# Performance work log

Measured on AMD Instinct MI355X. Metric: run time of the kernel, lower is better.

The kernel has to match this reference:

```python
import jax, jax.numpy as jnp
import numpy as np

B, C, H, W = 32, 64, 56, 56
REPN, NK, SMALL = 50, 17, 3   # repN=64-int(64*0.23), nk=ceil(51/3)
GROUPS = 4                     # N_rep
EPS = 1e-5


def _build_index_mats():
    """Reduce the fallback's python scatter-add loops to exact linear maps.
    For flat position p=r*NK+j the roll shifts depend only on p%3, so each
    shift class s gets a (REPN,NK) count matrix over source nk-slots."""
    rng = np.random.RandomState(123)
    ghost = np.sort(rng.choice(C, C - REPN, replace=False))
    rep = np.array(sorted(set(range(C)) - set(ghost.tolist())), np.int32)
    Mh = np.zeros((3, REPN, NK), np.int32)
    Mv = np.zeros((3, REPN, NK), np.int32)
    Mid = np.zeros((REPN, NK), np.int32)
    for _ in range(GROUPS):
        for r in range(REPN):
            perm = rng.permutation(NK)
            for p in range(NK):
                Mh[(r * NK + p) % 3, r, perm[p]] += 1
        for r in range(REPN):
            perm = rng.permutation(NK)
            for p in range(NK):
                Mv[(r * NK + p) % 3, r, perm[p]] += 1
        kk = rng.randint(0, NK, REPN)
        for r in range(REPN):
            Mid[r, kk[r]] += 1
    return ghost.astype(np.int32), rep, Mh, Mv, Mid


def setup_inputs() -> dict:
    key = jax.random.key(0)
    k1, k2, k3 = jax.random.split(key, 3)
    ghost, rep, Mh, Mv, Mid = _build_index_mats()
    return {
        "inputs": jax.random.normal(k1, (B, C, H, W), jnp.float32),
        "w0": jax.random.normal(k2, (REPN * NK, 1, SMALL, SMALL), jnp.float32) * 0.1,
        "w1": jax.random.normal(k3, (REPN * NK, 1, SMALL, SMALL), jnp.float32) * 0.1,
        "Mh": jnp.asarray(Mh), "Mv": jnp.asarray(Mv), "Mid": jnp.asarray(Mid),
        "ghost_idx": jnp.asarray(ghost), "rep_idx": jnp.asarray(rep),
    }


def _bn(x):
    # BatchNorm2d in training mode, affine weight=1 / bias=0 (init values)
    m = x.mean(axis=(0, 2, 3), keepdims=True)
    v = x.var(axis=(0, 2, 3), keepdims=True)
    return (x - m) / jnp.sqrt(v + EPS)


def reference(inputs, w0, w1, Mh, Mv, Mid, ghost_idx, rep_idx):
    rep_in = inputs[:, rep_idx]      # (B, REPN, H, W)
    ghost_in = inputs[:, ghost_idx]  # (B, ghostN, H, W)

    def conv(w):  # depthwise-grouped conv: groups=REPN, each 1->NK channels
        return jax.lax.conv_general_dilated(
            rep_in, w, window_strides=(1, 1), padding=((2, 2), (2, 2)),
            dimension_numbers=('NCHW', 'OIHW', 'NCHW'),
            feature_group_count=REPN)

    out = conv(w0) + conv(w1)                       # (B, REPN*NK, H+2, W+2)
    xv = out.reshape(B, REPN, NK, H + 2, W + 2)

    Mhf, Mvf, Midf = (m.astype(xv.dtype) for m in (Mh, Mv, Mid))
    sh1, sw1 = (0, 1, 2), (0, 2, 1)   # lora1: shifts (i%3, 2i%3)
    sh2, sw2 = (0, 2, 1), (0, 1, 2)   # lora2: shifts (2i%3, i%3)

    lora1 = sum(jnp.roll(jnp.einsum('rk,brkhw->brhw', Mhf[s], xv),
                         (sh1[s], sw1[s]), axis=(2, 3)) for s in range(3))
    lora2 = sum(jnp.roll(jnp.einsum('rk,brkhw->brhw', Mvf[s], xv),
                         (sh2[s], sw2[s]), axis=(2, 3)) for s in range(3))
    small = jnp.einsum('rk,brkhw->brhw', Midf, xv)

    # center-crop back to (H, W): dh = dw = 1
    lora1 = lora1[:, :, 1:1 + H, 1:1 + W]
    lora2 = lora2[:, :, 1:1 + H, 1:1 + W]
    small = small[:, :, 1:1 + H, 1:1 + W]

    x = _bn(lora1) + _bn(lora2) + _bn(small) + rep_in
    return jnp.concatenate([x, ghost_in], axis=1)   # (B, C, H, W)
```

## Files before the change

kernel.cpp:

```cpp
#include <hip/hip_runtime.h>
#include <hip/hip_cooperative_groups.h>

namespace cg = cooperative_groups;

#define Bn 32
#define Cn 64
#define Hn 56
#define Wn 56
#define REPN 50
#define NKn 17
#define HWn (Hn*Wn)
#define NSTATf 100352.0f
#define EPSf 1e-5f

#define PART_OFF 0
#define WEFF_OFF 9600

#define SEGH 7
#define NTASK 112

__device__ __forceinline__ void weff_one(int idx,
        const float* __restrict__ w0, const float* __restrict__ w1,
        const int* __restrict__ Mh, const int* __restrict__ Mv,
        const int* __restrict__ Mid, float* __restrict__ ws)
{
    int r   = idx / 63;
    int rem = idx % 63;
    int t   = rem / 9;
    int ij  = rem % 9;
    const int* M = (t < 3) ? (Mh + (t*REPN + r)*NKn)
                 : (t < 6) ? (Mv + ((t-3)*REPN + r)*NKn)
                           : (Mid + r*NKn);
    float acc = 0.f;
    #pragma unroll
    for (int k = 0; k < NKn; ++k)
        acc += (float)M[k] * (w0[(r*NKn + k)*9 + ij] + w1[(r*NKn + k)*9 + ij]);
    ws[WEFF_OFF + idx] = acc;
}

__global__ void k_weff(const float* __restrict__ w0, const float* __restrict__ w1,
                       const int* __restrict__ Mh, const int* __restrict__ Mv,
                       const int* __restrict__ Mid, float* __restrict__ ws)
{
    int idx = blockIdx.x * blockDim.x + threadIdx.x;
    if (idx < REPN*63) weff_one(idx, w0, w1, Mh, Mv, Mid, ws);
}

__device__ __forceinline__ void load_row8c(const float* __restrict__ ch, int row, int q,
                                           float* __restrict__ X, float& c55)
{
    bool rv = (row >= 0) && (row < Hn);
    int rc = rv ? row : 0;
    const float* rp = ch + rc*Wn;
    float4 c0 = *(const float4*)(rp + (q ? 4*q - 4 : 0));
    float4 c1 = *(const float4*)(rp + 4*q);
    int ox = (4*q + 4 <= 55) ? 4*q + 4 : 55;
    float cx = rp[ox];
    float mr = rv ? 1.f : 0.f;
    float m0 = (rv && q > 0)  ? 1.f : 0.f;
    float mx = (rv && q < 13) ? 1.f : 0.f;
    X[0]=c0.y*m0; X[1]=c0.z*m0; X[2]=c0.w*m0;
    X[3]=c1.x*mr; X[4]=c1.y*mr; X[5]=c1.z*mr; X[6]=c1.w*mr;
    X[7]=cx*mx;
    c55 = (q == 0) ? rp[55]*mr : 0.f;
}

template <typename F>
__device__ __forceinline__ void conv_walk(const float* __restrict__ ch,
        const float (&wk)[63], int tid, F emit)
{
    if (tid >= NTASK) return;
    int seg = tid / 14;
    int q   = tid - seg*14;
    int h0  = seg * SEGH;
    bool top = (seg == 0);

    float W[5][8], C[5], T[8];
    {
        float dummy;
        if (top) load_row8c(ch, 55, q, T, dummy);
    }
    #pragma unroll
    for (int k = 0; k < 5; ++k)
        load_row8c(ch, h0 - 3 + k, q, W[k], C[k]);

    #pragma unroll
    for (int s = 0; s < SEGH; ++s) {
        int h = h0 + s;
        float Wn8[8], Cn1;
        load_row8c(ch, h + 2, q, Wn8, Cn1);

        float l1[4], l2[4], sm[4];
        #pragma unroll
        for (int p = 0; p < 4; ++p) { l1[p]=0.f; l2[p]=0.f; sm[p]=0.f; }
        #pragma unroll
        for (int i = 0; i < 3; ++i)
            #pragma unroll
            for (int j = 0; j < 3; ++j) {
                float wh0 = wk[i*3+j],    wv0 = wk[27+i*3+j], wid = wk[54+i*3+j];
                float wh1 = wk[9+i*3+j],  wv2 = wk[45+i*3+j];
                float wh2 = wk[18+i*3+j], wv1 = wk[36+i*3+j];
                #pragma unroll
                for (int p = 0; p < 4; ++p) {
                    float a  = W[2+i][p+2+j];
                    l1[p] = fmaf(a, wh0, l1[p]);
                    l2[p] = fmaf(a, wv0, l2[p]);
                    sm[p] = fmaf(a, wid, sm[p]);
                    float bA = W[1+i][p+j];
                    l1[p] = fmaf(bA, wh1, l1[p]);
                    l2[p] = fmaf(bA, wv2, l2[p]);
                    float bB = W[i][p+1+j];
                    l1[p] = fmaf(bB, wh2, l1[p]);
                    l2[p] = fmaf(bB, wv1, l2[p]);
                }
            }
        if (q == 0) {
            #pragma unroll
            for (int i = 0; i < 3; ++i) {
                l1[0] = fmaf(C[1+i], wk[9+3*i],  l1[0]);
                l2[0] = fmaf(C[1+i], wk[45+3*i], l2[0]);
            }
        }
        if (s == 0 && top) {
            #pragma unroll
            for (int j = 0; j < 3; ++j)
                #pragma unroll
                for (int p = 0; p < 4; ++p) {
                    l1[p] = fmaf(T[p+1+j], wk[18+j], l1[p]);
                    l2[p] = fmaf(T[p+1+j], wk[36+j], l2[p]);
                }
        }
        float res[4] = {W[3][3], W[3][4], W[3][5], W[3][6]};
        emit(h, q, l1, l2, sm, res);

        #pragma unroll
        for (int k = 0; k < 4; ++k) {
            #pragma unroll
            for (int x = 0; x < 8; ++x) W[k][x] = W[k+1][x];
            C[k] = C[k+1];
        }
        #pragma unroll
        for (int x = 0; x < 8; ++x) W[4][x] = Wn8[x];
        C[4] = Cn1;
    }
}

__global__ void __launch_bounds__(128, 2) k_fused(const float* __restrict__ in,
        const float* __restrict__ w0, const float* __restrict__ w1,
        const int* __restrict__ Mh, const int* __restrict__ Mv,
        const int* __restrict__ Mid,
        const int* __restrict__ rep_idx, const int* __restrict__ ghost_idx,
        float* __restrict__ ws, float* __restrict__ out)
{
    cg::grid_group grid = cg::this_grid();
    int tid = threadIdx.x;

    {
        int gidx = blockIdx.x * 128 + tid;
        if (gidx < REPN*63) weff_one(gidx, w0, w1, Mh, Mv, Mid, ws);
    }
    grid.sync();

    __shared__ float red[2][6];
    #pragma unroll
    for (int it = 0; it < 2; ++it) {
        int v = blockIdx.x*2 + it;
        int c = v & 63;
        int b = v >> 6;
        if (c >= REPN) {
            int cin = ghost_idx[c - REPN];
            const float4* s4 = (const float4*)(in + ((size_t)(b*Cn + cin))*HWn);
            float4* d4 = (float4*)(out + ((size_t)(b*Cn + c))*HWn);
            for (int i = tid; i < HWn/4; i += 128) d4[i] = s4[i];
            continue;
        }
        int r = c;
        const float* wr = ws + WEFF_OFF + r*63;
        float wk[63];
        #pragma unroll
        for (int i = 0; i < 63; ++i) wk[i] = wr[i];
        const float* ch = in + ((size_t)(b*Cn + rep_idx[r]))*HWn;

        float s1=0.f,q1=0.f,s2=0.f,q2=0.f,s3=0.f,q3=0.f;
        conv_walk(ch, wk, tid,
            [&](int h, int q, float* l1, float* l2, float* sm, float* res) {
                (void)h; (void)q; (void)res;
                #pragma unroll
                for (int p = 0; p < 4; ++p) {
                    s1 += l1[p]; q1 += l1[p]*l1[p];
                    s2 += l2[p]; q2 += l2[p]*l2[p];
                    s3 += sm[p]; q3 += sm[p]*sm[p];
                }
            });
        __syncthreads();
        {
            float vals[6] = {s1,q1,s2,q2,s3,q3};
            int lane = tid & 63, wave = tid >> 6;
            #pragma unroll
            for (int x = 0; x < 6; ++x) {
                float y = vals[x];
                for (int o = 32; o; o >>= 1) y += __shfl_down(y, o, 64);
                if (lane == 0) red[wave][x] = y;
            }
        }
        __syncthreads();
        if (tid < 6)
            ws[PART_OFF + (tid*REPN + r)*Bn + b] = red[0][tid] + red[1][tid];
    }
    grid.sync();

    __shared__ float sred[6];
    #pragma unroll
    for (int it = 0; it < 2; ++it) {
        int v = blockIdx.x*2 + it;
        int c = v & 63;
        int b = v >> 6;
        if (c >= REPN) continue;
        int r = c;
        __syncthreads();
        if (tid < 6) {
            const float* pp = ws + PART_OFF + (tid*REPN + r)*Bn;
            float s = 0.f;
            #pragma unroll
            for (int i = 0; i < Bn; ++i) s += pp[i];
            sred[tid] = s;
        }
        __syncthreads();
        const float inv = 1.0f / NSTATf;
        float m1 = sred[0]*inv, v1 = sred[1]*inv - m1*m1;
        float m2 = sred[2]*inv, v2 = sred[3]*inv - m2*m2;
        float m3 = sred[4]*inv, v3 = sred[5]*inv - m3*m3;
        float r1 = rsqrtf(v1 + EPSf), r2 = rsqrtf(v2 + EPSf), r3 = rsqrtf(v3 + EPSf);

        const float* wr = ws + WEFF_OFF + r*63;
        float wk[63];
        #pragma unroll
        for (int i = 0; i < 63; ++i) wk[i] = wr[i];
        const float* ch = in + ((size_t)(b*Cn + rep_idx[r]))*HWn;
        float* dst = out + ((size_t)(b*Cn + c))*HWn;

        conv_walk(ch, wk, tid,
            [&](int h, int q, float* l1, float* l2, float* sm, float* res) {
                float4 o;
                o.x = (l1[0]-m1)*r1 + (l2[0]-m2)*r2 + (sm[0]-m3)*r3 + res[0];
                o.y = (l1[1]-m1)*r1 + (l2[1]-m2)*r2 + (sm[1]-m3)*r3 + res[1];
                o.z = (l1[2]-m1)*r1 + (l2[2]-m2)*r2 + (sm[2]-m3)*r3 + res[2];
                o.w = (l1[3]-m1)*r1 + (l2[3]-m2)*r2 + (sm[3]-m3)*r3 + res[3];
                *(float4*)(dst + h*Wn + 4*q) = o;
            });
    }
}

__global__ void __launch_bounds__(128) k_stats(const float* __restrict__ in,
        const int* __restrict__ rep_idx, float* __restrict__ ws)
{
    int bid = blockIdx.x;
    int r = bid % REPN;
    int b = bid / REPN;
    int tid = threadIdx.x;

    const float* wr = ws + WEFF_OFF + r*63;
    float wk[63];
    #pragma unroll
    for (int i = 0; i < 63; ++i) wk[i] = wr[i];
    const float* ch = in + ((size_t)(b*Cn + rep_idx[r]))*HWn;

    float s1=0.f,q1=0.f,s2=0.f,q2=0.f,s3=0.f,q3=0.f;
    conv_walk(ch, wk, tid,
        [&](int h, int q, float* l1, float* l2, float* sm, float* res) {
            (void)h; (void)q; (void)res;
            #pragma unroll
            for (int p = 0; p < 4; ++p) {
                s1 += l1[p]; q1 += l1[p]*l1[p];
                s2 += l2[p]; q2 += l2[p]*l2[p];
                s3 += sm[p]; q3 += sm[p]*sm[p];
            }
        });

    __shared__ float red[2][6];
    float vals[6] = {s1,q1,s2,q2,s3,q3};
    int lane = tid & 63, wave = tid >> 6;
    #pragma unroll
    for (int v = 0; v < 6; ++v) {
        float x = vals[v];
        for (int o = 32; o; o >>= 1) x += __shfl_down(x, o, 64);
        if (lane == 0) red[wave][v] = x;
    }
    __syncthreads();
    if (tid < 6)
        ws[PART_OFF + (tid*REPN + r)*Bn + b] = red[0][tid] + red[1][tid];
}

__global__ void __launch_bounds__(128) k_out(const float* __restrict__ in,
        const int* __restrict__ rep_idx, const int* __restrict__ ghost_idx,
        const float* __restrict__ ws, float* __restrict__ out)
{
    int bid = blockIdx.x;
    int c = bid % Cn;
    int b = bid / Cn;
    int tid = threadIdx.x;

    if (c >= REPN) {
        int cin = ghost_idx[c - REPN];
        const float4* s4 = (const float4*)(in + ((size_t)(b*Cn + cin))*HWn);
        float4* d4 = (float4*)(out + ((size_t)(b*Cn + c))*HWn);
        for (int i = tid; i < HWn/4; i += 128) d4[i] = s4[i];
        return;
    }

    int r = c;
    __shared__ float sred[6];
    if (tid < 6) {
        const float* pp = ws + PART_OFF + (tid*REPN + r)*Bn;
        float s = 0.f;
        #pragma unroll
        for (int i = 0; i < Bn; ++i) s += pp[i];
        sred[tid] = s;
    }
    __syncthreads();
    const float inv = 1.0f / NSTATf;
    float m1 = sred[0]*inv, v1 = sred[1]*inv - m1*m1;
    float m2 = sred[2]*inv, v2 = sred[3]*inv - m2*m2;
    float m3 = sred[4]*inv, v3 = sred[5]*inv - m3*m3;
    float r1 = rsqrtf(v1 + EPSf), r2 = rsqrtf(v2 + EPSf), r3 = rsqrtf(v3 + EPSf);

    const float* wr = ws + WEFF_OFF + r*63;
    float wk[63];
    #pragma unroll
    for (int i = 0; i < 63; ++i) wk[i] = wr[i];
    const float* ch = in + ((size_t)(b*Cn + rep_idx[r]))*HWn;
    float* dst = out + ((size_t)(b*Cn + c))*HWn;

    conv_walk(ch, wk, tid,
        [&](int h, int q, float* l1, float* l2, float* sm, float* res) {
            float4 o;
            o.x = (l1[0]-m1)*r1 + (l2[0]-m2)*r2 + (sm[0]-m3)*r3 + res[0];
            o.y = (l1[1]-m1)*r1 + (l2[1]-m2)*r2 + (sm[1]-m3)*r3 + res[1];
            o.z = (l1[2]-m1)*r1 + (l2[2]-m2)*r2 + (sm[2]-m3)*r3 + res[2];
            o.w = (l1[3]-m1)*r1 + (l2[3]-m2)*r2 + (sm[3]-m3)*r3 + res[3];
            *(float4*)(dst + h*Wn + 4*q) = o;
        });
}

extern "C" void kernel_launch(void* const* d_in, const int* in_sizes, int n_in,
                              void* d_out, int out_size, void* d_ws, size_t ws_size,
                              hipStream_t stream) {
    const float* in   = (const float*)d_in[0];
    const float* w0   = (const float*)d_in[1];
    const float* w1   = (const float*)d_in[2];
    const int*   Mh   = (const int*)d_in[3];
    const int*   Mv   = (const int*)d_in[4];
    const int*   Mid  = (const int*)d_in[5];
    const int*   ghost= (const int*)d_in[6];
    const int*   rep  = (const int*)d_in[7];
    float* out  = (float*)d_out;
    float* ws   = (float*)d_ws;

    int maxBlk = 0;
    hipError_t qerr = hipOccupancyMaxActiveBlocksPerMultiprocessor(
        &maxBlk, (const void*)k_fused, 128, 0);
    bool coop_ok = (qerr == hipSuccess) && (maxBlk >= 4);

    if (coop_ok) {
        void* args[] = { (void*)&in, (void*)&w0, (void*)&w1, (void*)&Mh,
                         (void*)&Mv, (void*)&Mid, (void*)&rep, (void*)&ghost,
                         (void*)&ws, (void*)&out };
        hipError_t lerr = hipLaunchCooperativeKernel((const void*)k_fused,
                              dim3(1024), dim3(128), args, 0, stream);
        if (lerr == hipSuccess) return;
    }
    k_weff<<<(REPN*63 + 127)/128, 128, 0, stream>>>(w0, w1, Mh, Mv, Mid, ws);
    k_stats<<<Bn*REPN, 128, 0, stream>>>(in, rep, ws);
    k_out<<<Bn*Cn, 128, 0, stream>>>(in, rep, ghost, ws, out);
}
```

Baseline: 124.2 us.

## Move folded conv weights to shared memory and launch one block per plane

Repacks the effective 3x3 weights into a padded 8-wide interleaved layout in shared memory, read as float4 pairs, instead of holding 63 weights in registers. This cuts register pressure so launch bounds can rise to 4 blocks per SIMD group, and the cooperative grid doubles to 2048 blocks, one (batch, channel) plane each. Ghost-channel copies now run before the first grid sync. The cost is LDS reads inside the inner loop and a stricter occupancy requirement (8 blocks per CU) for the cooperative path, otherwise it falls back to three separate kernels.

```diff
diff --git a/kernel.cpp b/kernel.cpp
--- a/kernel.cpp
+++ b/kernel.cpp
@@ -15,19 +15,22 @@
 
 #define PART_OFF 0
 #define WEFF_OFF 9600
+#define WEFF_N   (REPN*72)
 
 #define SEGH 7
 #define NTASK 112
+#define GRID_FUSED 2048
 
 __device__ __forceinline__ void weff_one(int idx,
         const float* __restrict__ w0, const float* __restrict__ w1,
         const int* __restrict__ Mh, const int* __restrict__ Mv,
         const int* __restrict__ Mid, float* __restrict__ ws)
 {
-    int r   = idx / 63;
-    int rem = idx % 63;
-    int t   = rem / 9;
-    int ij  = rem % 9;
+    int r   = idx / 72;
+    int rem = idx % 72;
+    int ij  = rem >> 3;
+    int t   = rem & 7;
+    if (t == 7) { ws[WEFF_OFF + idx] = 0.f; return; }
     const int* M = (t < 3) ? (Mh + (t*REPN + r)*NKn)
                  : (t < 6) ? (Mv + ((t-3)*REPN + r)*NKn)
                            : (Mid + r*NKn);
@@ -43,7 +46,7 @@
                        const int* __restrict__ Mid, float* __restrict__ ws)
 {
     int idx = blockIdx.x * blockDim.x + threadIdx.x;
-    if (idx < REPN*63) weff_one(idx, w0, w1, Mh, Mv, Mid, ws);
+    if (idx < WEFF_N) weff_one(idx, w0, w1, Mh, Mv, Mid, ws);
 }
 
 __device__ __forceinline__ void load_row8c(const float* __restrict__ ch, int row, int q,
@@ -67,7 +70,7 @@
 
 template <typename F>
 __device__ __forceinline__ void conv_walk(const float* __restrict__ ch,
-        const float (&wk)[63], int tid, F emit)
+        const float* __restrict__ swk, int tid, F emit)
 {
     if (tid >= NTASK) return;
     int seg = tid / 14;
@@ -90,6 +93,10 @@
         float Wn8[8], Cn1;
         load_row8c(ch, h + 2, q, Wn8, Cn1);
 
+        int z = 0;
+        asm volatile("" : "+v"(z));
+        const float* wz = swk + z;
+
         float l1[4], l2[4], sm[4];
         #pragma unroll
         for (int p = 0; p < 4; ++p) { l1[p]=0.f; l2[p]=0.f; sm[p]=0.f; }
@@ -97,9 +104,11 @@
         for (int i = 0; i < 3; ++i)
             #pragma unroll
             for (int j = 0; j < 3; ++j) {
-                float wh0 = wk[i*3+j],    wv0 = wk[27+i*3+j], wid = wk[54+i*3+j];
-                float wh1 = wk[9+i*3+j],  wv2 = wk[45+i*3+j];
-                float wh2 = wk[18+i*3+j], wv1 = wk[36+i*3+j];
+                int ij = i*3 + j;
+                float4 wa = *(const float4*)(wz + ij*8);
+                float4 wb = *(const float4*)(wz + ij*8 + 4);
+                float wh0 = wa.x, wh1 = wa.y, wh2 = wa.z, wv0 = wa.w;
+                float wv1 = wb.x, wv2 = wb.y, wid = wb.z;
                 #pragma unroll
                 for (int p = 0; p < 4; ++p) {
                     float a  = W[2+i][p+2+j];
@@ -117,8 +126,8 @@
         if (q == 0) {
             #pragma unroll
             for (int i = 0; i < 3; ++i) {
-                l1[0] = fmaf(C[1+i], wk[9+3*i],  l1[0]);
-                l2[0] = fmaf(C[1+i], wk[45+3*i], l2[0]);
+                l1[0] = fmaf(C[1+i], wz[(3*i)*8 + 1], l1[0]);
+                l2[0] = fmaf(C[1+i], wz[(3*i)*8 + 5], l2[0]);
             }
         }
         if (s == 0 && top) {
@@ -126,8 +135,8 @@
             for (int j = 0; j < 3; ++j)
                 #pragma unroll
                 for (int p = 0; p < 4; ++p) {
-                    l1[p] = fmaf(T[p+1+j], wk[18+j], l1[p]);
-                    l2[p] = fmaf(T[p+1+j], wk[36+j], l2[p]);
+                    l1[p] = fmaf(T[p+1+j], wz[j*8 + 2], l1[p]);
+                    l2[p] = fmaf(T[p+1+j], wz[j*8 + 4], l2[p]);
                 }
         }
         float res[4] = {W[3][3], W[3][4], W[3][5], W[3][6]};
@@ -145,7 +154,7 @@
     }
 }
 
-__global__ void __launch_bounds__(128, 2) k_fused(const float* __restrict__ in,
+__global__ void __launch_bounds__(128, 4) k_fused(const float* __restrict__ in,
         const float* __restrict__ w0, const float* __restrict__ w1,
         const int* __restrict__ Mh, const int* __restrict__ Mv,
         const int* __restrict__ Mid,
@@ -154,35 +163,35 @@
 {
     cg::grid_group grid = cg::this_grid();
     int tid = threadIdx.x;
+    int v = blockIdx.x;
+    int c = v & 63;
+    int b = v >> 6;
+    bool ghost = (c >= REPN);
+
+    __shared__ float swk[72];
+    __shared__ float red[2][6];
+    __shared__ float sred[6];
 
     {
         int gidx = blockIdx.x * 128 + tid;
-        if (gidx < REPN*63) weff_one(gidx, w0, w1, Mh, Mv, Mid, ws);
+        if (gidx < WEFF_N) weff_one(gidx, w0, w1, Mh, Mv, Mid, ws);
+    }
+    if (ghost) {
+        int cin = ghost_idx[c - REPN];
+        const float4* s4 = (const float4*)(in + ((size_t)(b*Cn + cin))*HWn);
+        float4* d4 = (float4*)(out + ((size_t)(b*Cn + c))*HWn);
+        for (int i = tid; i < HWn/4; i += 128) d4[i] = s4[i];
     }
     grid.sync();
 
-    __shared__ float red[2][6];
-    #pragma unroll
-    for (int it = 0; it < 2; ++it) {
-        int v = blockIdx.x*2 + it;
-        int c = v & 63;
-        int b = v >> 6;
-        if (c >= REPN) {
-            int cin = ghost_idx[c - REPN];
-            const float4* s4 = (const float4*)(in + ((size_t)(b*Cn + cin))*HWn);
-            float4* d4 = (float4*)(out + ((size_t)(b*Cn + c))*HWn);
-            for (int i = tid; i < HWn/4; i += 128) d4[i] = s4[i];
-            continue;
-        }
+    if (!ghost) {
         int r = c;
-        const float* wr = ws + WEFF_OFF + r*63;
-        float wk[63];
-        #pragma unroll
-        for (int i = 0; i < 63; ++i) wk[i] = wr[i];
+        if (tid < 72) swk[tid] = ws[WEFF_OFF + r*72 + tid];
+        __syncthreads();
         const float* ch = in + ((size_t)(b*Cn + rep_idx[r]))*HWn;
 
         float s1=0.f,q1=0.f,s2=0.f,q2=0.f,s3=0.f,q3=0.f;
-        conv_walk(ch, wk, tid,
+        conv_walk(ch, swk, tid,
             [&](int h, int q, float* l1, float* l2, float* sm, float* res) {
                 (void)h; (void)q; (void)res;
                 #pragma unroll
@@ -192,7 +201,6 @@
                     s3 += sm[p]; q3 += sm[p]*sm[p];
                 }
             });
-        __syncthreads();
         {
             float vals[6] = {s1,q1,s2,q2,s3,q3};
             int lane = tid & 63, wave = tid >> 6;
@@ -205,50 +213,38 @@
         }
         __syncthreads();
         if (tid < 6)
-            ws[PART_OFF + (tid*REPN + r)*Bn + b] = red[0][tid] + red[1][tid];
+            ws[PART_OFF + (tid*REPN + c)*Bn + b] = red[0][tid] + red[1][tid];
     }
     grid.sync();
 
-    __shared__ float sred[6];
-    #pragma unroll
-    for (int it = 0; it < 2; ++it) {
-        int v = blockIdx.x*2 + it;
-        int c = v & 63;
-        int b = v >> 6;
-        if (c >= REPN) continue;
-        int r = c;
-        __syncthreads();
-        if (tid < 6) {
-            const float* pp = ws + PART_OFF + (tid*REPN + r)*Bn;
-            float s = 0.f;
-            #pragma unroll
-            for (int i = 0; i < Bn; ++i) s += pp[i];
-            sred[tid] = s;
-        }
-        __syncthreads();
-        const float inv = 1.0f / NSTATf;
-        float m1 = sred[0]*inv, v1 = sred[1]*inv - m1*m1;
-        float m2 = sred[2]*inv, v2 = sred[3]*inv - m2*m2;
-        float m3 = sred[4]*inv, v3 = sred[5]*inv - m3*m3;
-        float r1 = rsqrtf(v1 + EPSf), r2 = rsqrtf(v2 + EPSf), r3 = rsqrtf(v3 + EPSf);
-
-        const float* wr = ws + WEFF_OFF + r*63;
-        float wk[63];
-        #pragma unroll
-        for (int i = 0; i < 63; ++i) wk[i] = wr[i];
-        const float* ch = in + ((size_t)(b*Cn + rep_idx[r]))*HWn;
-        float* dst = out + ((size_t)(b*Cn + c))*HWn;
-
-        conv_walk(ch, wk, tid,
-            [&](int h, int q, float* l1, float* l2, float* sm, float* res) {
-                float4 o;
-                o.x = (l1[0]-m1)*r1 + (l2[0]-m2)*r2 + (sm[0]-m3)*r3 + res[0];
-                o.y = (l1[1]-m1)*r1 + (l2[1]-m2)*r2 + (sm[1]-m3)*r3 + res[1];
-                o.z = (l1[2]-m1)*r1 + (l2[2]-m2)*r2 + (sm[2]-m3)*r3 + res[2];
-                o.w = (l1[3]-m1)*r1 + (l2[3]-m2)*r2 + (sm[3]-m3)*r3 + res[3];
-                *(float4*)(dst + h*Wn + 4*q) = o;
-            });
-    }
+    if (ghost) return;
+    int r = c;
+    if (tid < 6) {
+        const float* pp = ws + PART_OFF + (tid*REPN + r)*Bn;
+        float s = 0.f;
+        #pragma unroll
+        for (int i = 0; i < Bn; ++i) s += pp[i];
+        sred[tid] = s;
+    }
+    __syncthreads();
+    const float inv = 1.0f / NSTATf;
+    float m1 = sred[0]*inv, v1 = sred[1]*inv - m1*m1;
+    float m2 = sred[2]*inv, v2 = sred[3]*inv - m2*m2;
+    float m3 = sred[4]*inv, v3 = sred[5]*inv - m3*m3;
+    float r1 = rsqrtf(v1 + EPSf), r2 = rsqrtf(v2 + EPSf), r3 = rsqrtf(v3 + EPSf);
+
+    const float* ch = in + ((size_t)(b*Cn + rep_idx[r]))*HWn;
+    float* dst = out + ((size_t)(b*Cn + c))*HWn;
+
+    conv_walk(ch, swk, tid,
+        [&](int h, int q, float* l1, float* l2, float* sm, float* res) {
+            float4 o;
+            o.x = (l1[0]-m1)*r1 + (l2[0]-m2)*r2 + (sm[0]-m3)*r3 + res[0];
+            o.y = (l1[1]-m1)*r1 + (l2[1]-m2)*r2 + (sm[1]-m3)*r3 + res[1];
+            o.z = (l1[2]-m1)*r1 + (l2[2]-m2)*r2 + (sm[2]-m3)*r3 + res[2];
+            o.w = (l1[3]-m1)*r1 + (l2[3]-m2)*r2 + (sm[3]-m3)*r3 + res[3];
+            *(float4*)(dst + h*Wn + 4*q) = o;
+        });
 }
 
 __global__ void __launch_bounds__(128) k_stats(const float* __restrict__ in,
@@ -259,14 +255,13 @@
     int b = bid / REPN;
     int tid = threadIdx.x;
 
-    const float* wr = ws + WEFF_OFF + r*63;
-    float wk[63];
-    #pragma unroll
-    for (int i = 0; i < 63; ++i) wk[i] = wr[i];
+    __shared__ float swk[72];
+    if (tid < 72) swk[tid] = ws[WEFF_OFF + r*72 + tid];
+    __syncthreads();
     const float* ch = in + ((size_t)(b*Cn + rep_idx[r]))*HWn;
 
     float s1=0.f,q1=0.f,s2=0.f,q2=0.f,s3=0.f,q3=0.f;
-    conv_walk(ch, wk, tid,
+    conv_walk(ch, swk, tid,
         [&](int h, int q, float* l1, float* l2, float* sm, float* res) {
             (void)h; (void)q; (void)res;
             #pragma unroll
@@ -309,7 +304,9 @@
     }
 
     int r = c;
+    __shared__ float swk[72];
     __shared__ float sred[6];
+    if (tid < 72) swk[tid] = ws[WEFF_OFF + r*72 + tid];
     if (tid < 6) {
         const float* pp = ws + PART_OFF + (tid*REPN + r)*Bn;
         float s = 0.f;
@@ -324,14 +321,10 @@
     float m3 = sred[4]*inv, v3 = sred[5]*inv - m3*m3;
     float r1 = rsqrtf(v1 + EPSf), r2 = rsqrtf(v2 + EPSf), r3 = rsqrtf(v3 + EPSf);
 
-    const float* wr = ws + WEFF_OFF + r*63;
-    float wk[63];
-    #pragma unroll
-    for (int i = 0; i < 63; ++i) wk[i] = wr[i];
     const float* ch = in + ((size_t)(b*Cn + rep_idx[r]))*HWn;
     float* dst = out + ((size_t)(b*Cn + c))*HWn;
 
-    conv_walk(ch, wk, tid,
+    conv_walk(ch, swk, tid,
         [&](int h, int q, float* l1, float* l2, float* sm, float* res) {
             float4 o;
             o.x = (l1[0]-m1)*r1 + (l2[0]-m2)*r2 + (sm[0]-m3)*r3 + res[0];
@@ -359,17 +352,17 @@
     int maxBlk = 0;
     hipError_t qerr = hipOccupancyMaxActiveBlocksPerMultiprocessor(
         &maxBlk, (const void*)k_fused, 128, 0);
-    bool coop_ok = (qerr == hipSuccess) && (maxBlk >= 4);
+    bool coop_ok = (qerr == hipSuccess) && (maxBlk >= 8);
 
     if (coop_ok) {
         void* args[] = { (void*)&in, (void*)&w0, (void*)&w1, (void*)&Mh,
                          (void*)&Mv, (void*)&Mid, (void*)&rep, (void*)&ghost,
                          (void*)&ws, (void*)&out };
         hipError_t lerr = hipLaunchCooperativeKernel((const void*)k_fused,
-                              dim3(1024), dim3(128), args, 0, stream);
+                              dim3(GRID_FUSED), dim3(128), args, 0, stream);
         if (lerr == hipSuccess) return;
     }
-    k_weff<<<(REPN*63 + 127)/128, 128, 0, stream>>>(w0, w1, Mh, Mv, Mid, ws);
+    k_weff<<<(WEFF_N + 127)/128, 128, 0, stream>>>(w0, w1, Mh, Mv, Mid, ws);
     k_stats<<<Bn*REPN, 128, 0, stream>>>(in, rep, ws);
     k_out<<<Bn*Cn, 128, 0, stream>>>(in, rep, ghost, ws, out);
 }
```

Measured after the change: 133.4 us. +7.4%, slower.

## Replace cooperative kernel with two passes and fold BN into combined conv weights

Applied to the files above, without the earlier changes.

Removes the cooperative grid-synced kernel and its separate weight-combination pass. Each block now computes its own effective 3x3 weights into shared memory. The output pass folds the three batch-norm scalings into a single set of three shifted-kernel weights plus a constant, so it runs one convolution accumulation instead of three. This trades grid-wide syncs and one extra launch for redundant per-block weight computation and two regular launches, and it cuts the FMA count in the output pass.

```diff
diff --git a/kernel.cpp b/kernel.cpp
--- a/kernel.cpp
+++ b/kernel.cpp
@@ -1,7 +1,4 @@
 #include <hip/hip_runtime.h>
-#include <hip/hip_cooperative_groups.h>
-
-namespace cg = cooperative_groups;
 
 #define Bn 32
 #define Cn 64
@@ -14,36 +11,26 @@
 #define EPSf 1e-5f
 
 #define PART_OFF 0
-#define WEFF_OFF 9600
 
 #define SEGH 7
 #define NTASK 112
 
-__device__ __forceinline__ void weff_one(int idx,
+__device__ __forceinline__ void block_weff(int r, int tid,
         const float* __restrict__ w0, const float* __restrict__ w1,
         const int* __restrict__ Mh, const int* __restrict__ Mv,
-        const int* __restrict__ Mid, float* __restrict__ ws)
-{
-    int r   = idx / 63;
-    int rem = idx % 63;
-    int t   = rem / 9;
-    int ij  = rem % 9;
-    const int* M = (t < 3) ? (Mh + (t*REPN + r)*NKn)
-                 : (t < 6) ? (Mv + ((t-3)*REPN + r)*NKn)
-                           : (Mid + r*NKn);
-    float acc = 0.f;
-    #pragma unroll
-    for (int k = 0; k < NKn; ++k)
-        acc += (float)M[k] * (w0[(r*NKn + k)*9 + ij] + w1[(r*NKn + k)*9 + ij]);
-    ws[WEFF_OFF + idx] = acc;
-}
-
-__global__ void k_weff(const float* __restrict__ w0, const float* __restrict__ w1,
-                       const int* __restrict__ Mh, const int* __restrict__ Mv,
-                       const int* __restrict__ Mid, float* __restrict__ ws)
-{
-    int idx = blockIdx.x * blockDim.x + threadIdx.x;
-    if (idx < REPN*63) weff_one(idx, w0, w1, Mh, Mv, Mid, ws);
+        const int* __restrict__ Mid, float* __restrict__ swk)
+{
+    if (tid < 63) {
+        int t = tid / 9, ij = tid - t*9;
+        const int* M = (t < 3) ? (Mh + (t*REPN + r)*NKn)
+                     : (t < 6) ? (Mv + ((t-3)*REPN + r)*NKn)
+                               : (Mid + r*NKn);
+        float acc = 0.f;
+        #pragma unroll
+        for (int k = 0; k < NKn; ++k)
+            acc += (float)M[k] * (w0[(r*NKn + k)*9 + ij] + w1[(r*NKn + k)*9 + ij]);
+        swk[t*9 + ij] = acc;
+    }
 }
 
 __device__ __forceinline__ void load_row8c(const float* __restrict__ ch, int row, int q,
@@ -66,7 +53,7 @@
 }
 
 template <typename F>
-__device__ __forceinline__ void conv_walk(const float* __restrict__ ch,
+__device__ __forceinline__ void conv_walk3(const float* __restrict__ ch,
         const float (&wk)[63], int tid, F emit)
 {
     if (tid >= NTASK) return;
@@ -97,9 +84,10 @@
         for (int i = 0; i < 3; ++i)
             #pragma unroll
             for (int j = 0; j < 3; ++j) {
-                float wh0 = wk[i*3+j],    wv0 = wk[27+i*3+j], wid = wk[54+i*3+j];
-                float wh1 = wk[9+i*3+j],  wv2 = wk[45+i*3+j];
-                float wh2 = wk[18+i*3+j], wv1 = wk[36+i*3+j];
+                int ij = i*3 + j;
+                float wh0 = wk[ij],    wh1 = wk[9+ij],  wh2 = wk[18+ij];
+                float wv0 = wk[27+ij], wv1 = wk[36+ij], wv2 = wk[45+ij];
+                float wid = wk[54+ij];
                 #pragma unroll
                 for (int p = 0; p < 4; ++p) {
                     float a  = W[2+i][p+2+j];
@@ -145,113 +133,82 @@
     }
 }
 
-__global__ void __launch_bounds__(128, 2) k_fused(const float* __restrict__ in,
+__device__ __forceinline__ void conv_walk1(const float* __restrict__ ch,
+        const float (&cw0)[9], const float (&cwA)[9], const float (&cwB)[9],
+        float Kc, int tid, float* __restrict__ dst)
+{
+    if (tid >= NTASK) return;
+    int seg = tid / 14;
+    int q   = tid - seg*14;
+    int h0  = seg * SEGH;
+    bool top = (seg == 0);
+
+    float W[5][8], C[5], T[8];
+    {
+        float dummy;
+        if (top) load_row8c(ch, 55, q, T, dummy);
+    }
+    #pragma unroll
+    for (int k = 0; k < 5; ++k)
+        load_row8c(ch, h0 - 3 + k, q, W[k], C[k]);
+
+    #pragma unroll
+    for (int s = 0; s < SEGH; ++s) {
+        int h = h0 + s;
+        float Wn8[8], Cn1;
+        load_row8c(ch, h + 2, q, Wn8, Cn1);
+
+        float acc[4];
+        #pragma unroll
+        for (int p = 0; p < 4; ++p) acc[p] = 0.f;
+        #pragma unroll
+        for (int i = 0; i < 3; ++i)
+            #pragma unroll
+            for (int j = 0; j < 3; ++j) {
+                int ij = i*3 + j;
+                float w0c = cw0[ij], wAc = cwA[ij], wBc = cwB[ij];
+                #pragma unroll
+                for (int p = 0; p < 4; ++p) {
+                    acc[p] = fmaf(W[2+i][p+2+j], w0c, acc[p]);
+                    acc[p] = fmaf(W[1+i][p+j],   wAc, acc[p]);
+                    acc[p] = fmaf(W[i][p+1+j],   wBc, acc[p]);
+                }
+            }
+        if (q == 0) {
+            #pragma unroll
+            for (int i = 0; i < 3; ++i)
+                acc[0] = fmaf(C[1+i], cwA[3*i], acc[0]);
+        }
+        if (s == 0 && top) {
+            #pragma unroll
+            for (int j = 0; j < 3; ++j)
+                #pragma unroll
+                for (int p = 0; p < 4; ++p)
+                    acc[p] = fmaf(T[p+1+j], cwB[j], acc[p]);
+        }
+        float4 o;
+        o.x = acc[0] - Kc + W[3][3];
+        o.y = acc[1] - Kc + W[3][4];
+        o.z = acc[2] - Kc + W[3][5];
+        o.w = acc[3] - Kc + W[3][6];
+        *(float4*)(dst + h*Wn + 4*q) = o;
+
+        #pragma unroll
+        for (int k = 0; k < 4; ++k) {
+            #pragma unroll
+            for (int x = 0; x < 8; ++x) W[k][x] = W[k+1][x];
+            C[k] = C[k+1];
+        }
+        #pragma unroll
+        for (int x = 0; x < 8; ++x) W[4][x] = Wn8[x];
+        C[4] = Cn1;
+    }
+}
+
+__global__ void __launch_bounds__(128) k_pass1(const float* __restrict__ in,
         const float* __restrict__ w0, const float* __restrict__ w1,
         const int* __restrict__ Mh, const int* __restrict__ Mv,
         const int* __restrict__ Mid,
-        const int* __restrict__ rep_idx, const int* __restrict__ ghost_idx,
-        float* __restrict__ ws, float* __restrict__ out)
-{
-    cg::grid_group grid = cg::this_grid();
-    int tid = threadIdx.x;
-
-    {
-        int gidx = blockIdx.x * 128 + tid;
-        if (gidx < REPN*63) weff_one(gidx, w0, w1, Mh, Mv, Mid, ws);
-    }
-    grid.sync();
-
-    __shared__ float red[2][6];
-    #pragma unroll
-    for (int it = 0; it < 2; ++it) {
-        int v = blockIdx.x*2 + it;
-        int c = v & 63;
-        int b = v >> 6;
-        if (c >= REPN) {
-            int cin = ghost_idx[c - REPN];
-            const float4* s4 = (const float4*)(in + ((size_t)(b*Cn + cin))*HWn);
-            float4* d4 = (float4*)(out + ((size_t)(b*Cn + c))*HWn);
-            for (int i = tid; i < HWn/4; i += 128) d4[i] = s4[i];
-            continue;
-        }
-        int r = c;
-        const float* wr = ws + WEFF_OFF + r*63;
-        float wk[63];
-        #pragma unroll
-        for (int i = 0; i < 63; ++i) wk[i] = wr[i];
-        const float* ch = in + ((size_t)(b*Cn + rep_idx[r]))*HWn;
-
-        float s1=0.f,q1=0.f,s2=0.f,q2=0.f,s3=0.f,q3=0.f;
-        conv_walk(ch, wk, tid,
-            [&](int h, int q, float* l1, float* l2, float* sm, float* res) {
-                (void)h; (void)q; (void)res;
-                #pragma unroll
-                for (int p = 0; p < 4; ++p) {
-                    s1 += l1[p]; q1 += l1[p]*l1[p];
-                    s2 += l2[p]; q2 += l2[p]*l2[p];
-                    s3 += sm[p]; q3 += sm[p]*sm[p];
-                }
-            });
-        __syncthreads();
-        {
-            float vals[6] = {s1,q1,s2,q2,s3,q3};
-            int lane = tid & 63, wave = tid >> 6;
-            #pragma unroll
-            for (int x = 0; x < 6; ++x) {
-                float y = vals[x];
-                for (int o = 32; o; o >>= 1) y += __shfl_down(y, o, 64);
-                if (lane == 0) red[wave][x] = y;
-            }
-        }
-        __syncthreads();
-        if (tid < 6)
-            ws[PART_OFF + (tid*REPN + r)*Bn + b] = red[0][tid] + red[1][tid];
-    }
-    grid.sync();
-
-    __shared__ float sred[6];
-    #pragma unroll
-    for (int it = 0; it < 2; ++it) {
-        int v = blockIdx.x*2 + it;
-        int c = v & 63;
-        int b = v >> 6;
-        if (c >= REPN) continue;
-        int r = c;
-        __syncthreads();
-        if (tid < 6) {
-            const float* pp = ws + PART_OFF + (tid*REPN + r)*Bn;
-            float s = 0.f;
-            #pragma unroll
-            for (int i = 0; i < Bn; ++i) s += pp[i];
-            sred[tid] = s;
-        }
-        __syncthreads();
-        const float inv = 1.0f / NSTATf;
-        float m1 = sred[0]*inv, v1 = sred[1]*inv - m1*m1;
-        float m2 = sred[2]*inv, v2 = sred[3]*inv - m2*m2;
-        float m3 = sred[4]*inv, v3 = sred[5]*inv - m3*m3;
-        float r1 = rsqrtf(v1 + EPSf), r2 = rsqrtf(v2 + EPSf), r3 = rsqrtf(v3 + EPSf);
-
-        const float* wr = ws + WEFF_OFF + r*63;
-        float wk[63];
-        #pragma unroll
-        for (int i = 0; i < 63; ++i) wk[i] = wr[i];
-        const float* ch = in + ((size_t)(b*Cn + rep_idx[r]))*HWn;
-        float* dst = out + ((size_t)(b*Cn + c))*HWn;
-
-        conv_walk(ch, wk, tid,
-            [&](int h, int q, float* l1, float* l2, float* sm, float* res) {
-                float4 o;
-                o.x = (l1[0]-m1)*r1 + (l2[0]-m2)*r2 + (sm[0]-m3)*r3 + res[0];
-                o.y = (l1[1]-m1)*r1 + (l2[1]-m2)*r2 + (sm[1]-m3)*r3 + res[1];
-                o.z = (l1[2]-m1)*r1 + (l2[2]-m2)*r2 + (sm[2]-m3)*r3 + res[2];
-                o.w = (l1[3]-m1)*r1 + (l2[3]-m2)*r2 + (sm[3]-m3)*r3 + res[3];
-                *(float4*)(dst + h*Wn + 4*q) = o;
-            });
-    }
-}
-
-__global__ void __launch_bounds__(128) k_stats(const float* __restrict__ in,
         const int* __restrict__ rep_idx, float* __restrict__ ws)
 {
     int bid = blockIdx.x;
@@ -259,14 +216,19 @@
     int b = bid / REPN;
     int tid = threadIdx.x;
 
-    const float* wr = ws + WEFF_OFF + r*63;
+    __shared__ float swk[63];
+    __shared__ float red[2][6];
+
+    block_weff(r, tid, w0, w1, Mh, Mv, Mid, swk);
+    __syncthreads();
     float wk[63];
     #pragma unroll
-    for (int i = 0; i < 63; ++i) wk[i] = wr[i];
+    for (int i = 0; i < 63; ++i) wk[i] = swk[i];
+
     const float* ch = in + ((size_t)(b*Cn + rep_idx[r]))*HWn;
 
     float s1=0.f,q1=0.f,s2=0.f,q2=0.f,s3=0.f,q3=0.f;
-    conv_walk(ch, wk, tid,
+    conv_walk3(ch, wk, tid,
         [&](int h, int q, float* l1, float* l2, float* sm, float* res) {
             (void)h; (void)q; (void)res;
             #pragma unroll
@@ -277,27 +239,29 @@
             }
         });
 
-    __shared__ float red[2][6];
     float vals[6] = {s1,q1,s2,q2,s3,q3};
     int lane = tid & 63, wave = tid >> 6;
     #pragma unroll
-    for (int v = 0; v < 6; ++v) {
-        float x = vals[v];
-        for (int o = 32; o; o >>= 1) x += __shfl_down(x, o, 64);
-        if (lane == 0) red[wave][v] = x;
+    for (int x = 0; x < 6; ++x) {
+        float y = vals[x];
+        for (int o = 32; o; o >>= 1) y += __shfl_down(y, o, 64);
+        if (lane == 0) red[wave][x] = y;
     }
     __syncthreads();
     if (tid < 6)
         ws[PART_OFF + (tid*REPN + r)*Bn + b] = red[0][tid] + red[1][tid];
 }
 
-__global__ void __launch_bounds__(128) k_out(const float* __restrict__ in,
+__global__ void __launch_bounds__(128) k_pass2(const float* __restrict__ in,
+        const float* __restrict__ w0, const float* __restrict__ w1,
+        const int* __restrict__ Mh, const int* __restrict__ Mv,
+        const int* __restrict__ Mid,
         const int* __restrict__ rep_idx, const int* __restrict__ ghost_idx,
         const float* __restrict__ ws, float* __restrict__ out)
 {
     int bid = blockIdx.x;
-    int c = bid % Cn;
-    int b = bid / Cn;
+    int c = bid & 63;
+    int b = bid >> 6;
     int tid = threadIdx.x;
 
     if (c >= REPN) {
@@ -307,39 +271,40 @@
         for (int i = tid; i < HWn/4; i += 128) d4[i] = s4[i];
         return;
     }
-
     int r = c;
+
+    __shared__ float swk[63];
     __shared__ float sred[6];
-    if (tid < 6) {
-        const float* pp = ws + PART_OFF + (tid*REPN + r)*Bn;
+
+    block_weff(r, tid, w0, w1, Mh, Mv, Mid, swk);
+    if (tid >= 64 && tid < 70) {
+        int x = tid - 64;
+        const float* pp = ws + PART_OFF + (x*REPN + r)*Bn;
         float s = 0.f;
         #pragma unroll
         for (int i = 0; i < Bn; ++i) s += pp[i];
-        sred[tid] = s;
+        sred[x] = s;
     }
     __syncthreads();
+
     const float inv = 1.0f / NSTATf;
     float m1 = sred[0]*inv, v1 = sred[1]*inv - m1*m1;
     float m2 = sred[2]*inv, v2 = sred[3]*inv - m2*m2;
     float m3 = sred[4]*inv, v3 = sred[5]*inv - m3*m3;
     float r1 = rsqrtf(v1 + EPSf), r2 = rsqrtf(v2 + EPSf), r3 = rsqrtf(v3 + EPSf);
-
-    const float* wr = ws + WEFF_OFF + r*63;
-    float wk[63];
-    #pragma unroll
-    for (int i = 0; i < 63; ++i) wk[i] = wr[i];
+    float Kc = m1*r1 + m2*r2 + m3*r3;
+
+    float cw0[9], cwA[9], cwB[9];
+    #pragma unroll
+    for (int ij = 0; ij < 9; ++ij) {
+        cw0[ij] = r1*swk[ij]      + r2*swk[27+ij] + r3*swk[54+ij];
+        cwA[ij] = r1*swk[9+ij]    + r2*swk[45+ij];
+        cwB[ij] = r1*swk[18+ij]   + r2*swk[36+ij];
+    }
+
     const float* ch = in + ((size_t)(b*Cn + rep_idx[r]))*HWn;
     float* dst = out + ((size_t)(b*Cn + c))*HWn;
-
-    conv_walk(ch, wk, tid,
-        [&](int h, int q, float* l1, float* l2, float* sm, float* res) {
-            float4 o;
-            o.x = (l1[0]-m1)*r1 + (l2[0]-m2)*r2 + (sm[0]-m3)*r3 + res[0];
-            o.y = (l1[1]-m1)*r1 + (l2[1]-m2)*r2 + (sm[1]-m3)*r3 + res[1];
-            o.z = (l1[2]-m1)*r1 + (l2[2]-m2)*r2 + (sm[2]-m3)*r3 + res[2];
-            o.w = (l1[3]-m1)*r1 + (l2[3]-m2)*r2 + (sm[3]-m3)*r3 + res[3];
-            *(float4*)(dst + h*Wn + 4*q) = o;
-        });
+    conv_walk1(ch, cw0, cwA, cwB, Kc, tid, dst);
 }
 
 extern "C" void kernel_launch(void* const* d_in, const int* in_sizes, int n_in,
@@ -356,20 +321,6 @@
     float* out  = (float*)d_out;
     float* ws   = (float*)d_ws;
 
-    int maxBlk = 0;
-    hipError_t qerr = hipOccupancyMaxActiveBlocksPerMultiprocessor(
-        &maxBlk, (const void*)k_fused, 128, 0);
-    bool coop_ok = (qerr == hipSuccess) && (maxBlk >= 4);
-
-    if (coop_ok) {
-        void* args[] = { (void*)&in, (void*)&w0, (void*)&w1, (void*)&Mh,
-                         (void*)&Mv, (void*)&Mid, (void*)&rep, (void*)&ghost,
-                         (void*)&ws, (void*)&out };
-        hipError_t lerr = hipLaunchCooperativeKernel((const void*)k_fused,
-                              dim3(1024), dim3(128), args, 0, stream);
-        if (lerr == hipSuccess) return;
-    }
-    k_weff<<<(REPN*63 + 127)/128, 128, 0, stream>>>(w0, w1, Mh, Mv, Mid, ws);
-    k_stats<<<Bn*REPN, 128, 0, stream>>>(in, rep, ws);
-    k_out<<<Bn*Cn, 128, 0, stream>>>(in, rep, ghost, ws, out);
-}
+    k_pass1<<<REPN*Bn, 128, 0, stream>>>(in, w0, w1, Mh, Mv, Mid, rep, ws);
+    k_pass2<<<Bn*Cn,   128, 0, stream>>>(in, w0, w1, Mh, Mv, Mid, rep, ghost, ws, out);
+}
```

After: 121.4 us. -2.3%, faster.
